# Kernel optimization log

Measured on AMD Instinct MI355X. Metric: run time of the kernel, lower is better.

## Reference

```python
import jax, jax.numpy as jnp
import numpy as np

D_MODEL = 1024
N_HEADS = 16
HEAD_DIM = D_MODEL // N_HEADS
SEQ = 4096
BATCH = 4


def setup_inputs() -> dict:
    key = jax.random.key(0)
    ks = jax.random.split(key, 10)
    s = 0.02
    inp = {
        "h": jax.random.normal(ks[0], (SEQ, BATCH, D_MODEL), jnp.float32),
        "x": jax.random.normal(ks[1], (SEQ, BATCH, D_MODEL), jnp.float32),
        "Wq": jax.random.normal(ks[2], (D_MODEL, D_MODEL), jnp.float32) * s,
        "bq": jnp.zeros((D_MODEL,), jnp.float32),
        "Wk": jax.random.normal(ks[3], (D_MODEL, D_MODEL), jnp.float32) * s,
        "bk": jnp.zeros((D_MODEL,), jnp.float32),
        "Wv": jax.random.normal(ks[4], (D_MODEL, D_MODEL), jnp.float32) * s,
        "bv": jnp.zeros((D_MODEL,), jnp.float32),
        "Wo": jax.random.normal(ks[5], (D_MODEL, D_MODEL), jnp.float32) * s,
        "bo": jnp.zeros((D_MODEL,), jnp.float32),
    }
    return inp


def _heads(t):
    # [S, B, D] -> [B, H, S, d]
    S, B, _ = t.shape
    return t.reshape(S, B, N_HEADS, HEAD_DIM).transpose(1, 2, 0, 3)


def reference(h, x, Wq, bq, Wk, bk, Wv, bv, Wo, bo):
    # torch Linear: y = x @ W.T + b
    Q = _heads(h @ Wq.T + bq)
    K = _heads(x @ Wk.T + bk)
    V = _heads(x @ Wv.T + bv)
    Qp = jax.nn.elu(Q) + 1.0
    Kp = jax.nn.elu(K) + 1.0
    KV = jnp.einsum('bhsd,bhsv->bhdv', Kp, V)          # [B,H,d,d]
    K_sum = Kp.sum(axis=2)                              # [B,H,d]
    Z = jnp.einsum('bhsd,bhd->bhs', Qp, K_sum) + 1e-6   # [B,H,S]
    out = jnp.einsum('bhsd,bhdv->bhsv', Qp, KV) / Z[..., None]
    # [B,H,S,d] -> [S,B,D]
    S, B = h.shape[0], h.shape[1]
    out = out.transpose(2, 0, 1, 3).reshape(S, B, D_MODEL)
    return out @ Wo.T + bo
```

## Files before the change

### kernel.cpp

```cpp
#include <hip/hip_runtime.h>
#include <hip/hip_bf16.h>
#include <cstdint>
#include <cstddef>

#define S_LEN   4096
#define BATCHN  4
#define DMODEL  1024
#define NHEADS  16
#define HDIM    64
#define MROWS   (S_LEN*BATCHN)
#define KDIM    1024
#define KSPLIT  8
#define NTK     (KDIM/32)

typedef __bf16 bf16;
typedef bf16 bf16x8 __attribute__((ext_vector_type(8)));
typedef bf16 bf16x4 __attribute__((ext_vector_type(4)));
typedef float f32x4 __attribute__((ext_vector_type(4)));

#define MFMA16(a,b,c) __builtin_amdgcn_mfma_f32_16x16x32_bf16(a,b,c,0,0,0)

__device__ __forceinline__ void gll16(const void* g, void* l) {
  __builtin_amdgcn_global_load_lds((const __attribute__((address_space(1))) unsigned*)g,
                                   (__attribute__((address_space(3))) unsigned*)l,
                                   16, 0, 0);
}

__global__ __launch_bounds__(256) void cast_perm(const float* __restrict__ h,
                                                 const float* __restrict__ x,
                                                 bf16* __restrict__ hb,
                                                 bf16* __restrict__ xb) {
  const int n = MROWS * KDIM;
  int stride = gridDim.x * blockDim.x * 4;
  for (int i = (blockIdx.x * blockDim.x + threadIdx.x) * 4; i < n; i += stride) {
    int s = i >> 12, b = (i >> 10) & 3, d = i & 1023;
    size_t o = ((size_t)(b * S_LEN + s) << 10) | d;
    float4 f = *(const float4*)(h + i);
    bf16x4 u; u[0]=(bf16)f.x; u[1]=(bf16)f.y; u[2]=(bf16)f.z; u[3]=(bf16)f.w;
    *(bf16x4*)(hb + o) = u;
    float4 g = *(const float4*)(x + i);
    bf16x4 v; v[0]=(bf16)g.x; v[1]=(bf16)g.y; v[2]=(bf16)g.z; v[3]=(bf16)g.w;
    *(bf16x4*)(xb + o) = v;
  }
}

__global__ __launch_bounds__(256) void cast_w(const float* __restrict__ Wq,
                                              const float* __restrict__ Wk,
                                              const float* __restrict__ Wv,
                                              const float* __restrict__ Wo,
                                              bf16* __restrict__ dst) {
  const int n = 4 * 1048576;
  int stride = gridDim.x * blockDim.x * 4;
  for (int i = (blockIdx.x * blockDim.x + threadIdx.x) * 4; i < n; i += stride) {
    int r = i >> 20;
    const float* src = (r < 1) ? (Wq + i) : (r < 2) ? (Wk + i - 1048576)
                     : (r < 3) ? (Wv + i - 2097152) : (Wo + i - 3145728);
    float4 f = *(const float4*)src;
    bf16x4 o; o[0]=(bf16)f.x; o[1]=(bf16)f.y; o[2]=(bf16)f.z; o[3]=(bf16)f.w;
    *(bf16x4*)(dst + i) = o;
  }
}

struct GemmAcc { f32x4 a[4][4]; };

__device__ __forceinline__ void gemm_tile(const bf16* __restrict__ A,
                                          const bf16* __restrict__ Bw,
                                          size_t arow0, size_t brow0,
                                          bf16* sm, GemmAcc& G) {
  const int tid  = threadIdx.x;
  const int wid  = tid >> 6;
  const int lane = tid & 63;
  const int wm = wid >> 1, wn = wid & 1;
  const int lr = lane >> 2;
  const int lc = lane & 3;
  const int ssrc = (((lc << 4) ^ (((lr >> 1) & 3) << 4)) >> 1);
  const int fhalf = (lane >> 4) << 4;

  const bf16* ap[2]; const bf16* bp[2]; int sdo[2];
  #pragma unroll
  for (int i = 0; i < 2; ++i) {
    int seg = (wid << 1) | i;
    ap[i] = A  + (arow0 + seg*16 + lr) * KDIM + ssrc;
    bp[i] = Bw + (brow0 + seg*16 + lr) * KDIM + ssrc;
    sdo[i] = seg * 512;
  }

  #pragma unroll
  for (int i = 0; i < 2; ++i) { gll16(ap[i],      sm + sdo[i]); gll16(bp[i],      sm + 4096 + sdo[i]); }
  #pragma unroll
  for (int i = 0; i < 2; ++i) { gll16(ap[i] + 32, sm + 8192 + sdo[i]); gll16(bp[i] + 32, sm + 12288 + sdo[i]); }
  asm volatile("s_waitcnt vmcnt(4)" ::: "memory");
  __builtin_amdgcn_s_barrier();
  asm volatile("" ::: "memory");

  int cur = 0;
  for (int t = 0; t < NTK; ++t) {
    const bf16* As = sm + cur * 8192;
    const bf16* Bs = As + 4096;

    bf16x8 af[4], bfv[4];
    #pragma unroll
    for (int m = 0; m < 4; ++m) {
      int R = wm*64 + m*16 + (lane & 15);
      af[m] = *(const bf16x8*)((const char*)As + R*64 + (fhalf ^ (((R >> 1) & 3) << 4)));
    }
    #pragma unroll
    for (int n = 0; n < 4; ++n) {
      int R = wn*64 + n*16 + (lane & 15);
      bfv[n] = *(const bf16x8*)((const char*)Bs + R*64 + (fhalf ^ (((R >> 1) & 3) << 4)));
    }

    if (t + 2 < NTK) {
      int nx2 = cur + 2; if (nx2 >= 3) nx2 -= 3;
      bf16* wbA = sm + nx2 * 8192;
      const int ko = (t + 2) * 32;
      #pragma unroll
      for (int i = 0; i < 2; ++i) {
        gll16(ap[i] + ko, wbA + sdo[i]);
        gll16(bp[i] + ko, wbA + 4096 + sdo[i]);
      }
    }

    #pragma unroll
    for (int m = 0; m < 4; ++m)
      #pragma unroll
      for (int n = 0; n < 4; ++n)
        G.a[m][n] = MFMA16(af[m], bfv[n], G.a[m][n]);

    if (t < NTK - 2)       asm volatile("s_waitcnt vmcnt(4)" ::: "memory");
    else if (t == NTK - 2) asm volatile("s_waitcnt vmcnt(0)" ::: "memory");
    if (t < NTK - 1) {
      __builtin_amdgcn_s_barrier();
      asm volatile("" ::: "memory");
    }
    cur = (cur == 2) ? 0 : cur + 1;
  }
}

template<int MODE>
__global__ __launch_bounds__(256) void gemm_bt(
    const bf16* __restrict__ A, const bf16* __restrict__ Bw,
    const float* __restrict__ bias0, const float* __restrict__ bias1,
    void* __restrict__ Cout) {
  __shared__ __align__(16) bf16 sm[3 * 8192];
  const int tid  = threadIdx.x;
  const int wid  = tid >> 6;
  const int lane = tid & 63;
  const int wm = wid >> 1, wn = wid & 1;
  const int mtile = blockIdx.x, ntile = blockIdx.y;
  const int CP = (MODE == 1) ? MROWS : DMODEL;

  GemmAcc G = {};
  gemm_tile(A, Bw, (size_t)mtile * 128, (size_t)ntile * 128, sm, G);

  #pragma unroll
  for (int m = 0; m < 4; ++m) {
    int rowb = mtile*128 + wm*64 + m*16 + ((lane >> 4) << 2);
    #pragma unroll
    for (int n = 0; n < 4; ++n) {
      int col = ntile*128 + wn*64 + n*16 + (lane & 15);
      if (MODE == 0) {
        float bias = bias0[col];
        bf16* C = (bf16*)Cout;
        #pragma unroll
        for (int i = 0; i < 4; ++i) {
          float v = G.a[m][n][i] + bias;
          v = (v > 0.f) ? v + 1.f : __expf(v);
          C[(size_t)(rowb+i)*CP + col] = (bf16)v;
        }
      } else if (MODE == 1) {
        bf16* C = (bf16*)Cout;
        #pragma unroll
        for (int i = 0; i < 4; ++i) {
          int r = rowb + i;
          float v = G.a[m][n][i] + ((r < 1024) ? bias0[r] : bias1[r - 1024]);
          if (r < 1024) v = (v > 0.f) ? v + 1.f : __expf(v);
          C[(size_t)r*CP + col] = (bf16)v;
        }
      } else {
        float bias = bias0[col];
        float* C = (float*)Cout;
        #pragma unroll
        for (int i = 0; i < 4; ++i)
          C[(size_t)(rowb+i)*CP + col] = G.a[m][n][i] + bias;
      }
    }
  }
}

__global__ __launch_bounds__(256) void kv_gemm(const bf16* __restrict__ kvt,
                                               float* __restrict__ KVg,
                                               float* __restrict__ Ksumg) {
  const int bh = blockIdx.x;
  const int k0base = blockIdx.y * (S_LEN / KSPLIT);
  const int b = bh >> 4, hh = bh & 15;
  const int tid = threadIdx.x, wid = tid >> 6, lane = tid & 63;
  const int wm = wid >> 1, wn = wid & 1;
  __shared__ __align__(16) bf16 Ks[64*64];
  __shared__ __align__(16) bf16 Vs[64*64];
  const bf16* Kh = kvt + (size_t)(hh*64) * MROWS + b * S_LEN;
  const bf16* Vh = kvt + (size_t)(1024 + hh*64) * MROWS + b * S_LEN;
  f32x4 acc[2][2] = {};
  float ksl0 = 0.f, ksl1 = 0.f;

  for (int k0 = k0base; k0 < k0base + S_LEN/KSPLIT; k0 += 64) {
    #pragma unroll
    for (int j = 0; j < 4; ++j) {
      int cchunk = wid*4 + j;
      int r = (cchunk & 7) * 8 + (lane >> 3);
      int colb = (lane & 7) * 16;
      int scol = colb ^ ((r & 7) << 4);
      const bf16* src = (cchunk < 8) ? Kh : Vh;
      bf16* dst = ((cchunk < 8) ? Ks : Vs) + (size_t)(cchunk & 7) * 8 * 64;
      gll16(src + (size_t)r * MROWS + k0 + (scol >> 1), dst);
    }
    __syncthreads();
    #pragma unroll
    for (int ksb = 0; ksb < 2; ++ksb) {
      bf16x8 af[2], bv[2];
      #pragma unroll
      for (int m = 0; m < 2; ++m) {
        int R = wm*32 + m*16 + (lane & 15);
        int cb = (ksb*64 + ((lane >> 4) << 4)) ^ ((R & 7) << 4);
        af[m] = *(const bf16x8*)((const char*)Ks + R*128 + cb);
      }
      #pragma unroll
      for (int n = 0; n < 2; ++n) {
        int R = wn*32 + n*16 + (lane & 15);
        int cb = (ksb*64 + ((lane >> 4) << 4)) ^ ((R & 7) << 4);
        bv[n] = *(const bf16x8*)((const char*)Vs + R*128 + cb);
      }
      if (wn == 0) {
        #pragma unroll
        for (int j = 0; j < 8; ++j) { ksl0 += (float)af[0][j]; ksl1 += (float)af[1][j]; }
      }
      #pragma unroll
      for (int m = 0; m < 2; ++m)
        #pragma unroll
        for (int n = 0; n < 2; ++n)
          acc[m][n] = MFMA16(af[m], bv[n], acc[m][n]);
    }
    __syncthreads();
  }

  #pragma unroll
  for (int m = 0; m < 2; ++m)
    #pragma unroll
    for (int n = 0; n < 2; ++n)
      #pragma unroll
      for (int i = 0; i < 4; ++i) {
        int dd = wm*32 + m*16 + ((lane >> 4) << 2) + i;
        int vv = wn*32 + n*16 + (lane & 15);
        atomicAdd(&KVg[(size_t)bh*4096 + dd*64 + vv], acc[m][n][i]);
      }

  if (wn == 0) {
    float v0 = ksl0, v1 = ksl1;
    v0 += __shfl_xor(v0, 16); v0 += __shfl_xor(v0, 32);
    v1 += __shfl_xor(v1, 16); v1 += __shfl_xor(v1, 32);
    if (lane < 16) {
      atomicAdd(&Ksumg[bh*64 + wm*32 + lane], v0);
      atomicAdd(&Ksumg[bh*64 + wm*32 + 16 + lane], v1);
    }
  }
}

__global__ __launch_bounds__(256) void attn_out(const bf16* __restrict__ QP,
                                                const float* __restrict__ KVg,
                                                const float* __restrict__ Ksumg,
                                                bf16* __restrict__ OP) {
  const int head = blockIdx.x, stile = blockIdx.y;
  const int b = head >> 4, hh = head & 15;
  const int tid = threadIdx.x;
  const int wid = tid >> 6, lane = tid & 63;
  const int s0 = stile * 128;
  __shared__ __align__(16) bf16 Qs[128*64];
  __shared__ __align__(16) bf16 KVt[64*64];
  __shared__ float ksum_s[64];
  __shared__ float rZ[128];

  const float* KVh = KVg + (size_t)head*4096;
  #pragma unroll
  for (int i = 0; i < 16; ++i) {
    int idx = i*256 + tid;
    int dd = idx >> 6, vv = idx & 63;
    KVt[vv*64 + dd] = (bf16)KVh[idx];
  }
  if (tid < 64) ksum_s[tid] = Ksumg[head*64 + tid];
  #pragma unroll
  for (int p = 0; p < 4; ++p) {
    int row = p*32 + wid*8 + (lane >> 3);
    gll16(QP + ((size_t)(b*S_LEN + s0 + row))*DMODEL + hh*64 + ((lane&7)<<3),
          Qs + (p*32 + wid*8)*64);
  }
  __syncthreads();

  if (tid < 128) {
    float z = 0.f;
    #pragma unroll
    for (int dd = 0; dd < 64; ++dd) z += (float)Qs[tid*64 + dd] * ksum_s[dd];
    rZ[tid] = 1.f / (z + 1e-6f);
  }
  __syncthreads();

  f32x4 acc[2][4] = {};
  #pragma unroll
  for (int ksb = 0; ksb < 2; ++ksb) {
    bf16x8 af[2], bv[4];
    #pragma unroll
    for (int m = 0; m < 2; ++m)
      af[m] = *(const bf16x8*)(Qs + (wid*32 + m*16 + (lane & 15))*64 + ksb*32 + ((lane>>4)<<3));
    #pragma unroll
    for (int n = 0; n < 4; ++n)
      bv[n] = *(const bf16x8*)(KVt + (n*16 + (lane & 15))*64 + ksb*32 + ((lane>>4)<<3));
    #pragma unroll
    for (int m = 0; m < 2; ++m)
      #pragma unroll
      for (int n = 0; n < 4; ++n)
        acc[m][n] = MFMA16(af[m], bv[n], acc[m][n]);
  }

  #pragma unroll
  for (int m = 0; m < 2; ++m)
    #pragma unroll
    for (int n = 0; n < 4; ++n)
      #pragma unroll
      for (int i = 0; i < 4; ++i) {
        int row = wid*32 + m*16 + ((lane >> 4) << 2) + i;
        int vv  = n*16 + (lane & 15);
        float val = acc[m][n][i] * rZ[row];
        OP[((size_t)((s0+row)*BATCHN + b))*DMODEL + hh*64 + vv] = (bf16)val;
      }
}

extern "C" void kernel_launch(void* const* d_in, const int* in_sizes, int n_in,
                              void* d_out, int out_size, void* d_ws, size_t ws_size,
                              hipStream_t stream) {
  const float* h  = (const float*)d_in[0];
  const float* x  = (const float*)d_in[1];
  const float* Wq = (const float*)d_in[2];
  const float* bq = (const float*)d_in[3];
  const float* Wk = (const float*)d_in[4];
  const float* bk = (const float*)d_in[5];
  const float* Wv = (const float*)d_in[6];
  const float* bv = (const float*)d_in[7];
  const float* Wo = (const float*)d_in[8];
  const float* bo = (const float*)d_in[9];

  char* ws = (char*)d_ws;
  bf16*  hb   = (bf16*)(ws);
  bf16*  xb   = (bf16*)(ws + 33554432);
  bf16*  wcat = (bf16*)(ws + 67108864);
  bf16*  wob  = (bf16*)(ws + 73400320);
  bf16*  qp   = (bf16*)(ws + 75497472);
  bf16*  kvt  = (bf16*)(ws + 109051904);
  float* kvb  = (float*)(ws + 176160768);
  float* ksb  = (float*)(ws + 177209344);
  bf16*  op   = (bf16*)(ws + 177225728);

  cast_perm<<<dim3(4096), 256, 0, stream>>>(h, x, hb, xb);
  cast_w<<<dim3(2048), 256, 0, stream>>>(Wq, Wk, Wv, Wo, wcat);

  hipMemsetAsync(kvb, 0, 1048576 + 16384, stream);

  gemm_bt<1><<<dim3(16, 128), 256, 0, stream>>>(wcat + 1048576, xb, bk, bv, kvt);
  gemm_bt<0><<<dim3(128, 8),  256, 0, stream>>>(hb, wcat, bq, nullptr, qp);
  kv_gemm<<<dim3(64, KSPLIT), 256, 0, stream>>>(kvt, kvb, ksb);
  attn_out<<<dim3(64, 32), 256, 0, stream>>>(qp, kvb, ksb, op);
  gemm_bt<2><<<dim3(128, 8), 256, 0, stream>>>(op, wob, bo, nullptr, d_out);
}
```

Measured before the change: 266.8 us.

## Fuse K/V projection with per-tile KV outer product and K-sum

```diff
diff --git a/kernel.cpp b/kernel.cpp
--- a/kernel.cpp
+++ b/kernel.cpp
@@ -10,8 +10,8 @@
 #define HDIM    64
 #define MROWS   (S_LEN*BATCHN)
 #define KDIM    1024
-#define KSPLIT  8
 #define NTK     (KDIM/32)
+#define CLP     136
 
 typedef __bf16 bf16;
 typedef bf16 bf16x8 __attribute__((ext_vector_type(8)));
@@ -140,7 +140,7 @@
 template<int MODE>
 __global__ __launch_bounds__(256) void gemm_bt(
     const bf16* __restrict__ A, const bf16* __restrict__ Bw,
-    const float* __restrict__ bias0, const float* __restrict__ bias1,
+    const float* __restrict__ bias0,
     void* __restrict__ Cout) {
   __shared__ __align__(16) bf16 sm[3 * 8192];
   const int tid  = threadIdx.x;
@@ -148,7 +148,6 @@
   const int lane = tid & 63;
   const int wm = wid >> 1, wn = wid & 1;
   const int mtile = blockIdx.x, ntile = blockIdx.y;
-  const int CP = (MODE == 1) ? MROWS : DMODEL;
 
   GemmAcc G = {};
   gemm_tile(A, Bw, (size_t)mtile * 128, (size_t)ntile * 128, sm, G);
@@ -159,108 +158,159 @@
     #pragma unroll
     for (int n = 0; n < 4; ++n) {
       int col = ntile*128 + wn*64 + n*16 + (lane & 15);
+      float bias = bias0[col];
       if (MODE == 0) {
-        float bias = bias0[col];
         bf16* C = (bf16*)Cout;
         #pragma unroll
         for (int i = 0; i < 4; ++i) {
           float v = G.a[m][n][i] + bias;
           v = (v > 0.f) ? v + 1.f : __expf(v);
-          C[(size_t)(rowb+i)*CP + col] = (bf16)v;
-        }
-      } else if (MODE == 1) {
-        bf16* C = (bf16*)Cout;
-        #pragma unroll
-        for (int i = 0; i < 4; ++i) {
-          int r = rowb + i;
-          float v = G.a[m][n][i] + ((r < 1024) ? bias0[r] : bias1[r - 1024]);
-          if (r < 1024) v = (v > 0.f) ? v + 1.f : __expf(v);
-          C[(size_t)r*CP + col] = (bf16)v;
+          C[(size_t)(rowb+i)*DMODEL + col] = (bf16)v;
         }
       } else {
-        float bias = bias0[col];
         float* C = (float*)Cout;
         #pragma unroll
         for (int i = 0; i < 4; ++i)
-          C[(size_t)(rowb+i)*CP + col] = G.a[m][n][i] + bias;
+          C[(size_t)(rowb+i)*DMODEL + col] = G.a[m][n][i] + bias;
       }
     }
   }
 }
 
-__global__ __launch_bounds__(256) void kv_gemm(const bf16* __restrict__ kvt,
-                                               float* __restrict__ KVg,
-                                               float* __restrict__ Ksumg) {
-  const int bh = blockIdx.x;
-  const int k0base = blockIdx.y * (S_LEN / KSPLIT);
-  const int b = bh >> 4, hh = bh & 15;
-  const int tid = threadIdx.x, wid = tid >> 6, lane = tid & 63;
+__global__ __launch_bounds__(512, 4) void kvproj(
+    const bf16* __restrict__ Wkv, const bf16* __restrict__ xb,
+    const float* __restrict__ bk, const float* __restrict__ bv,
+    float* __restrict__ kvb, float* __restrict__ ksb) {
+  __shared__ __align__(16) bf16 sm[3 * 12288];
+  const int tid  = threadIdx.x;
+  const int wid  = tid >> 6;
+  const int lane = tid & 63;
   const int wm = wid >> 1, wn = wid & 1;
-  __shared__ __align__(16) bf16 Ks[64*64];
-  __shared__ __align__(16) bf16 Vs[64*64];
-  const bf16* Kh = kvt + (size_t)(hh*64) * MROWS + b * S_LEN;
-  const bf16* Vh = kvt + (size_t)(1024 + hh*64) * MROWS + b * S_LEN;
-  f32x4 acc[2][2] = {};
-  float ksl0 = 0.f, ksl1 = 0.f;
-
-  for (int k0 = k0base; k0 < k0base + S_LEN/KSPLIT; k0 += 64) {
-    #pragma unroll
-    for (int j = 0; j < 4; ++j) {
-      int cchunk = wid*4 + j;
-      int r = (cchunk & 7) * 8 + (lane >> 3);
-      int colb = (lane & 7) * 16;
-      int scol = colb ^ ((r & 7) << 4);
-      const bf16* src = (cchunk < 8) ? Kh : Vh;
-      bf16* dst = ((cchunk < 8) ? Ks : Vs) + (size_t)(cchunk & 7) * 8 * 64;
-      gll16(src + (size_t)r * MROWS + k0 + (scol >> 1), dst);
-    }
-    __syncthreads();
-    #pragma unroll
-    for (int ksb = 0; ksb < 2; ++ksb) {
-      bf16x8 af[2], bv[2];
-      #pragma unroll
-      for (int m = 0; m < 2; ++m) {
-        int R = wm*32 + m*16 + (lane & 15);
-        int cb = (ksb*64 + ((lane >> 4) << 4)) ^ ((R & 7) << 4);
-        af[m] = *(const bf16x8*)((const char*)Ks + R*128 + cb);
+  const int m = blockIdx.x, ntile = blockIdx.y;
+  const int lr = lane >> 2;
+  const int lc = lane & 3;
+  const int ssrc = (((lc << 4) ^ (((lr >> 1) & 3) << 4)) >> 1);
+  const int fhalf = (lane >> 4) << 4;
+
+  const bf16* KA = Wkv + (size_t)(m * 128) * KDIM;
+  const bf16* VA = Wkv + (size_t)(1024 + m * 128) * KDIM;
+  const bf16* BB = xb + (size_t)(ntile * 128) * KDIM;
+
+  const bf16* ap[2]; const bf16* bp; int sda[2], sdb;
+  #pragma unroll
+  for (int i = 0; i < 2; ++i) {
+    int seg = (wid << 1) | i;
+    const bf16* base = (seg < 8) ? KA : VA;
+    ap[i] = base + (size_t)((seg & 7) * 16 + lr) * KDIM + ssrc;
+    sda[i] = seg * 512;
+  }
+  bp = BB + (size_t)(wid * 16 + lr) * KDIM + ssrc;
+  sdb = 8192 + wid * 512;
+
+  #pragma unroll
+  for (int i = 0; i < 2; ++i) gll16(ap[i], sm + sda[i]);
+  gll16(bp, sm + sdb);
+  #pragma unroll
+  for (int i = 0; i < 2; ++i) gll16(ap[i] + 32, sm + 12288 + sda[i]);
+  gll16(bp + 32, sm + 12288 + sdb);
+  asm volatile("s_waitcnt vmcnt(3)" ::: "memory");
+  __builtin_amdgcn_s_barrier();
+  asm volatile("" ::: "memory");
+
+  f32x4 acc[4][4] = {};
+  int cur = 0;
+  for (int t = 0; t < NTK; ++t) {
+    const bf16* As = sm + cur * 12288;
+    const bf16* Bs = As + 8192;
+
+    bf16x8 af[4], bfv[4];
+    #pragma unroll
+    for (int mm = 0; mm < 4; ++mm) {
+      int R = wm*64 + mm*16 + (lane & 15);
+      af[mm] = *(const bf16x8*)((const char*)As + R*64 + (fhalf ^ (((R >> 1) & 3) << 4)));
+    }
+    #pragma unroll
+    for (int nn = 0; nn < 4; ++nn) {
+      int R = wn*64 + nn*16 + (lane & 15);
+      bfv[nn] = *(const bf16x8*)((const char*)Bs + R*64 + (fhalf ^ (((R >> 1) & 3) << 4)));
+    }
+
+    if (t + 2 < NTK) {
+      int nx2 = cur + 2; if (nx2 >= 3) nx2 -= 3;
+      bf16* wb = sm + nx2 * 12288;
+      const int ko = (t + 2) * 32;
+      #pragma unroll
+      for (int i = 0; i < 2; ++i) gll16(ap[i] + ko, wb + sda[i]);
+      gll16(bp + ko, wb + sdb);
+    }
+
+    #pragma unroll
+    for (int mm = 0; mm < 4; ++mm)
+      #pragma unroll
+      for (int nn = 0; nn < 4; ++nn)
+        acc[mm][nn] = MFMA16(af[mm], bfv[nn], acc[mm][nn]);
+
+    if (t < NTK - 2)       asm volatile("s_waitcnt vmcnt(3)" ::: "memory");
+    else if (t == NTK - 2) asm volatile("s_waitcnt vmcnt(0)" ::: "memory");
+    if (t < NTK - 1) {
+      __builtin_amdgcn_s_barrier();
+      asm volatile("" ::: "memory");
+    }
+    cur = (cur == 2) ? 0 : cur + 1;
+  }
+  __syncthreads();
+
+  bf16* CL = sm;
+  #pragma unroll
+  for (int mm = 0; mm < 4; ++mm) {
+    #pragma unroll
+    for (int i = 0; i < 4; ++i) {
+      int ra = wm*64 + mm*16 + ((lane >> 4) << 2) + i;
+      float bias = (ra < 128) ? bk[m*128 + ra] : bv[m*128 + ra - 128];
+      #pragma unroll
+      for (int nn = 0; nn < 4; ++nn) {
+        int cb = wn*64 + nn*16 + (lane & 15);
+        float v = acc[mm][nn][i] + bias;
+        if (ra < 128) v = (v > 0.f) ? v + 1.f : __expf(v);
+        CL[ra*CLP + cb] = (bf16)v;
       }
-      #pragma unroll
-      for (int n = 0; n < 2; ++n) {
-        int R = wn*32 + n*16 + (lane & 15);
-        int cb = (ksb*64 + ((lane >> 4) << 4)) ^ ((R & 7) << 4);
-        bv[n] = *(const bf16x8*)((const char*)Vs + R*128 + cb);
-      }
-      if (wn == 0) {
-        #pragma unroll
-        for (int j = 0; j < 8; ++j) { ksl0 += (float)af[0][j]; ksl1 += (float)af[1][j]; }
-      }
-      #pragma unroll
-      for (int m = 0; m < 2; ++m)
-        #pragma unroll
-        for (int n = 0; n < 2; ++n)
-          acc[m][n] = MFMA16(af[m], bv[n], acc[m][n]);
-    }
-    __syncthreads();
-  }
-
-  #pragma unroll
-  for (int m = 0; m < 2; ++m)
-    #pragma unroll
-    for (int n = 0; n < 2; ++n)
-      #pragma unroll
-      for (int i = 0; i < 4; ++i) {
-        int dd = wm*32 + m*16 + ((lane >> 4) << 2) + i;
-        int vv = wn*32 + n*16 + (lane & 15);
-        atomicAdd(&KVg[(size_t)bh*4096 + dd*64 + vv], acc[m][n][i]);
-      }
-
-  if (wn == 0) {
-    float v0 = ksl0, v1 = ksl1;
-    v0 += __shfl_xor(v0, 16); v0 += __shfl_xor(v0, 32);
-    v1 += __shfl_xor(v1, 16); v1 += __shfl_xor(v1, 32);
-    if (lane < 16) {
-      atomicAdd(&Ksumg[bh*64 + wm*32 + lane], v0);
-      atomicAdd(&Ksumg[bh*64 + wm*32 + 16 + lane], v1);
+    }
+  }
+  __syncthreads();
+
+  const int hl = wid >> 2;
+  const int ww = wid & 3;
+  const int bh = (ntile >> 5) * 16 + 2*m + hl;
+  f32x4 acc2[4] = {};
+  #pragma unroll
+  for (int ks = 0; ks < 4; ++ks) {
+    bf16x8 akv = *(const bf16x8*)(CL + (hl*64 + ww*16 + (lane & 15))*CLP + ks*32 + ((lane >> 4) << 3));
+    #pragma unroll
+    for (int nn = 0; nn < 4; ++nn) {
+      bf16x8 bkv = *(const bf16x8*)(CL + (128 + hl*64 + nn*16 + (lane & 15))*CLP + ks*32 + ((lane >> 4) << 3));
+      acc2[nn] = MFMA16(akv, bkv, acc2[nn]);
+    }
+  }
+  float* KVh = kvb + (size_t)bh * 4096;
+  #pragma unroll
+  for (int nn = 0; nn < 4; ++nn)
+    #pragma unroll
+    for (int i = 0; i < 4; ++i) {
+      int dd = ww*16 + ((lane >> 4) << 2) + i;
+      int vv = nn*16 + (lane & 15);
+      atomicAdd(&KVh[dd*64 + vv], acc2[nn][i]);
+    }
+
+  {
+    int rid = tid >> 2, part = tid & 3;
+    float s = 0.f;
+    #pragma unroll
+    for (int j = 0; j < 32; ++j) s += (float)CL[rid*CLP + part*32 + j];
+    s += __shfl_xor(s, 1);
+    s += __shfl_xor(s, 2);
+    if (part == 0) {
+      int hh = rid >> 6, d = rid & 63;
+      atomicAdd(&ksb[((ntile >> 5) * 16 + 2*m + hh)*64 + d], s);
     }
   }
 }
@@ -305,14 +355,14 @@
 
   f32x4 acc[2][4] = {};
   #pragma unroll
-  for (int ksb = 0; ksb < 2; ++ksb) {
+  for (int ksb2 = 0; ksb2 < 2; ++ksb2) {
     bf16x8 af[2], bv[4];
     #pragma unroll
     for (int m = 0; m < 2; ++m)
-      af[m] = *(const bf16x8*)(Qs + (wid*32 + m*16 + (lane & 15))*64 + ksb*32 + ((lane>>4)<<3));
+      af[m] = *(const bf16x8*)(Qs + (wid*32 + m*16 + (lane & 15))*64 + ksb2*32 + ((lane>>4)<<3));
     #pragma unroll
     for (int n = 0; n < 4; ++n)
-      bv[n] = *(const bf16x8*)(KVt + (n*16 + (lane & 15))*64 + ksb*32 + ((lane>>4)<<3));
+      bv[n] = *(const bf16x8*)(KVt + (n*16 + (lane & 15))*64 + ksb2*32 + ((lane>>4)<<3));
     #pragma unroll
     for (int m = 0; m < 2; ++m)
       #pragma unroll
@@ -353,19 +403,17 @@
   bf16*  wcat = (bf16*)(ws + 67108864);
   bf16*  wob  = (bf16*)(ws + 73400320);
   bf16*  qp   = (bf16*)(ws + 75497472);
-  bf16*  kvt  = (bf16*)(ws + 109051904);
-  float* kvb  = (float*)(ws + 176160768);
-  float* ksb  = (float*)(ws + 177209344);
-  bf16*  op   = (bf16*)(ws + 177225728);
+  float* kvb  = (float*)(ws + 109051904);
+  float* ksb  = (float*)(ws + 110100480);
+  bf16*  op   = (bf16*)(ws + 110116864);
 
   cast_perm<<<dim3(4096), 256, 0, stream>>>(h, x, hb, xb);
   cast_w<<<dim3(2048), 256, 0, stream>>>(Wq, Wk, Wv, Wo, wcat);
 
   hipMemsetAsync(kvb, 0, 1048576 + 16384, stream);
 
-  gemm_bt<1><<<dim3(16, 128), 256, 0, stream>>>(wcat + 1048576, xb, bk, bv, kvt);
-  gemm_bt<0><<<dim3(128, 8),  256, 0, stream>>>(hb, wcat, bq, nullptr, qp);
-  kv_gemm<<<dim3(64, KSPLIT), 256, 0, stream>>>(kvt, kvb, ksb);
+  kvproj<<<dim3(8, 128), 512, 0, stream>>>(wcat + 1048576, xb, bk, bv, kvb, ksb);
+  gemm_bt<0><<<dim3(128, 8), 256, 0, stream>>>(hb, wcat, bq, qp);
   attn_out<<<dim3(64, 32), 256, 0, stream>>>(qp, kvb, ksb, op);
-  gemm_bt<2><<<dim3(128, 8), 256, 0, stream>>>(op, wob, bo, nullptr, d_out);
-}
+  gemm_bt<2><<<dim3(128, 8), 256, 0, stream>>>(op, wob, bo, d_out);
+}
```

Result: faster. 257.1 us (-3.6%).
